# Performance work log

Measured on AMD Instinct MI355X. Metric: run time of the kernel, lower is better.

The kernel has to match this reference:

```python
import jax, jax.numpy as jnp
import numpy as np

N, C_IN, C_OUT = 8192, 256, 128
NEG_SLOPE = 0.2


def setup_inputs() -> dict:
    key = jax.random.key(0)
    k0, k1, k2, k3, k4 = jax.random.split(key, 5)
    x = jax.random.normal(k0, (N, C_IN), dtype=jnp.float32)
    # sparse-ish binary dense adjacency, avg degree ~32
    adj = (jax.random.uniform(k1, (N, N)) < (32.0 / N)).astype(jnp.float32)
    W = jax.random.normal(k2, (C_IN, C_OUT), dtype=jnp.float32) * 0.05
    att_src = jax.random.normal(k3, (C_OUT,), dtype=jnp.float32) * 0.1
    att_dst = jax.random.normal(k4, (C_OUT,), dtype=jnp.float32) * 0.1
    bias = jnp.zeros((C_OUT,), dtype=jnp.float32)
    return {"x": x, "adj": adj, "W": W, "att_src": att_src,
            "att_dst": att_dst, "bias": bias}


def reference(x, adj, W, att_src, att_dst, bias):
    n = adj.shape[0]
    idx = jnp.arange(n)
    adj = adj.at[idx, idx].set(1.0)          # add self loops
    h = x @ W                                 # [N, C_out]
    a_src = h @ att_src                       # [N]
    a_dst = h @ att_dst                       # [N]
    alpha = a_src[:, None] + a_dst[None, :]   # [N, N]
    alpha = jax.nn.leaky_relu(alpha, NEG_SLOPE)
    alpha = adj * jnp.exp(alpha)              # masked exp
    alpha = alpha / alpha.sum(axis=0, keepdims=True)  # column-normalize (dim=0)
    out = (adj * alpha).T @ h + bias          # [N, C_out]
    return out
```

## Files before the change

### kernel.cpp

```cpp
#include <hip/hip_runtime.h>
#include <hip/hip_bf16.h>

#define NN 8192
#define CIN 256
#define COUT 128
#define GR 32
#define GKT 64
#define CH 16
#define ICH (NN / CH)
#define KT 64
#define HTS 72

typedef unsigned short u16;
typedef _Float16 f16;
typedef __attribute__((ext_vector_type(8))) short short8;
typedef __attribute__((ext_vector_type(8))) _Float16 f16x8;
typedef __attribute__((ext_vector_type(16))) float f32x16;

__device__ __forceinline__ short8 pack8_bf16(const float* v) {
    union { __hip_bfloat162 b2[4]; short8 s; } u;
    #pragma unroll
    for (int q = 0; q < 4; ++q)
        u.b2[q] = __float22bfloat162_rn(make_float2(v[2 * q], v[2 * q + 1]));
    return u.s;
}

__global__ __launch_bounds__(256) void adj2mask(const float* __restrict__ adj,
                                                unsigned int* __restrict__ maskT) {
    int tid = threadIdx.x;
    int lane = tid & 63, w = tid >> 6;
    int i = blockIdx.x * 4 + w;
    const float4* rowp = (const float4*)(adj + (size_t)i * NN);
    int half = lane >> 5, slot = lane & 3;
    bool writer = (lane & 31) < 4;
    for (int it = 0; it < 32; it += 8) {
        float4 v[8];
        #pragma unroll
        for (int q = 0; q < 8; ++q)
            v[q] = rowp[(it + q) * 64 + lane];
        #pragma unroll
        for (int q = 0; q < 8; ++q) {
            unsigned long long b0 = __ballot(v[q].x != 0.f);
            unsigned long long b1 = __ballot(v[q].y != 0.f);
            unsigned long long b2 = __ballot(v[q].z != 0.f);
            unsigned long long b3 = __ballot(v[q].w != 0.f);
            unsigned long long bb = slot == 0 ? b0 : slot == 1 ? b1
                                  : slot == 2 ? b2 : b3;
            unsigned int mw = (unsigned int)(bb >> (half * 32));
            int jb = (it + q) * 2 + half;
            if (writer)
                maskT[((size_t)jb * NN + i) * 4 + slot] = mw;
        }
    }
}

__global__ __launch_bounds__(256) void gemm_h(const float* __restrict__ x,
                                              const float* __restrict__ W,
                                              const float* __restrict__ att_src,
                                              const float* __restrict__ att_dst,
                                              u16* __restrict__ h_t,
                                              float* __restrict__ a_src,
                                              float* __restrict__ a_dst) {
    __shared__ float Wt[GKT * COUT];
    __shared__ float xt[GKT][GR + 4];
    __shared__ float ot[GR][COUT + 4];
    int tid = threadIdx.x;
    int i0 = blockIdx.x * GR;
    int tx = tid & 31, ty = tid >> 5;
    int c0 = tx * 4, r0 = ty * 4;
    int xr = tid >> 3, xk = (tid & 7) * 8;
    float acc[4][4] = {};

    for (int kt = 0; kt < CIN; kt += GKT) {
        float4 wv[8];
        #pragma unroll
        for (int j = 0; j < 8; ++j) {
            int f = j * 256 + tid;
            wv[j] = *(const float4*)&W[(size_t)(kt + (f >> 5)) * COUT + (f & 31) * 4];
        }
        float4 xv0 = *(const float4*)&x[(size_t)(i0 + xr) * CIN + kt + xk];
        float4 xv1 = *(const float4*)&x[(size_t)(i0 + xr) * CIN + kt + xk + 4];
        __syncthreads();
        #pragma unroll
        for (int j = 0; j < 8; ++j)
            *(float4*)&Wt[(j * 256 + tid) * 4] = wv[j];
        xt[xk + 0][xr] = xv0.x; xt[xk + 1][xr] = xv0.y;
        xt[xk + 2][xr] = xv0.z; xt[xk + 3][xr] = xv0.w;
        xt[xk + 4][xr] = xv1.x; xt[xk + 5][xr] = xv1.y;
        xt[xk + 6][xr] = xv1.z; xt[xk + 7][xr] = xv1.w;
        __syncthreads();
        #pragma unroll 8
        for (int k = 0; k < GKT; ++k) {
            float4 wk = *(const float4*)&Wt[k * COUT + c0];
            float4 xf = *(const float4*)&xt[k][r0];
            float xa[4] = {xf.x, xf.y, xf.z, xf.w};
            #pragma unroll
            for (int a = 0; a < 4; ++a) {
                acc[a][0] += xa[a] * wk.x; acc[a][1] += xa[a] * wk.y;
                acc[a][2] += xa[a] * wk.z; acc[a][3] += xa[a] * wk.w;
            }
        }
    }

    float4 asv = *(const float4*)&att_src[c0];
    float4 adv = *(const float4*)&att_dst[c0];
    #pragma unroll
    for (int a = 0; a < 4; ++a) {
        float4 o = make_float4(acc[a][0], acc[a][1], acc[a][2], acc[a][3]);
        *(float4*)&ot[r0 + a][c0] = o;
        float s = o.x * asv.x + o.y * asv.y + o.z * asv.z + o.w * asv.w;
        float d = o.x * adv.x + o.y * adv.y + o.z * adv.z + o.w * adv.w;
        #pragma unroll
        for (int m = 16; m >= 1; m >>= 1) {
            s += __shfl_xor(s, m, 32);
            d += __shfl_xor(d, m, 32);
        }
        if (tx == 0) {
            a_src[i0 + r0 + a] = s;
            a_dst[i0 + r0 + a] = d;
        }
    }
    __syncthreads();
    int c = tid >> 1, hf = tid & 1;
    float vals[16];
    #pragma unroll
    for (int q = 0; q < 16; ++q) vals[q] = ot[hf * 16 + q][c];
    *(short8*)(h_t + (size_t)c * NN + i0 + hf * 16)     = pack8_bf16(vals);
    *(short8*)(h_t + (size_t)c * NN + i0 + hf * 16 + 8) = pack8_bf16(vals + 8);
}

__global__ __launch_bounds__(256, 3) void gat_mm(const unsigned int* __restrict__ maskT,
                                                 const u16* __restrict__ h_t,
                                                 const float* __restrict__ a_src,
                                                 const float* __restrict__ a_dst,
                                                 f16* __restrict__ pout,
                                                 float* __restrict__ pden) {
    __shared__ unsigned int maskS[KT * 4];
    __shared__ u16 htS[128 * HTS];
    __shared__ float asrcS[ICH];
    int tid = threadIdx.x;
    int lane = tid & 63, w = tid >> 6;
    int jb = blockIdx.x & 63, ch = blockIdx.x >> 6;
    int j0 = jb * 128;
    int i0 = ch * ICH;
    int half = lane >> 5;
    int jloc = w * 32 + (lane & 31);
    int gj = j0 + jloc;
    int slot = lane & 3;
    int kbit = jloc >> 2;
    float dj = a_dst[gj];
    if (tid < ICH / 4)
        ((float4*)asrcS)[tid] = ((const float4*)(a_src + i0))[tid];

    f32x16 acc[4];
    #pragma unroll
    for (int nt = 0; nt < 4; ++nt)
        #pragma unroll
        for (int q = 0; q < 16; ++q) acc[nt][q] = 0.f;
    float dsum = 0.f;
    __syncthreads();

    for (int s = 0; s < ICH / KT; ++s) {
        int ib = i0 + s * KT;
        unsigned int mword = maskT[((size_t)jb * NN + ib) * 4 + tid];
        short8 bv[4]; int bc[4], bi[4];
        #pragma unroll
        for (int q = 0; q < 4; ++q) {
            int p = q * 256 + tid;
            bc[q] = p >> 3; bi[q] = (p & 7) * 8;
            bv[q] = *(const short8*)(h_t + (size_t)bc[q] * NN + ib + bi[q]);
        }
        maskS[tid] = mword;
        #pragma unroll
        for (int q = 0; q < 4; ++q)
            *(short8*)(htS + bc[q] * HTS + bi[q]) = bv[q];
        __syncthreads();

        #pragma unroll
        for (int kk = 0; kk < 4; ++kk) {
            int kb = kk * 16 + half * 8;
            int gib = ib + kb;
            short8 bf[4];
            #pragma unroll
            for (int nt = 0; nt < 4; ++nt)
                bf[nt] = *(const short8*)(htS + (nt * 32 + (lane & 31)) * HTS + kb);
            float pv[8];
            #pragma unroll
            for (int e = 0; e < 8; ++e) {
                unsigned int mw = maskS[(kb + e) * 4 + slot];
                float t = asrcS[s * KT + kb + e] + dj;
                float ev = __expf(fmaxf(t, 0.2f * t));
                bool on = ((mw >> kbit) & 1u) | (gib + e == gj);
                pv[e] = on ? ev : 0.f;
                dsum += pv[e];
            }
            short8 af = pack8_bf16(pv);
            #pragma unroll
            for (int nt = 0; nt < 4; ++nt)
                acc[nt] = __builtin_amdgcn_mfma_f32_32x32x16_bf16(af, bf[nt],
                                                                  acc[nt], 0, 0, 0);
        }
        __syncthreads();
    }

    #pragma unroll
    for (int nt = 0; nt < 4; ++nt) {
        int c = nt * 32 + (lane & 31);
        #pragma unroll
        for (int r = 0; r < 16; ++r) {
            int row = (r & 3) + 8 * (r >> 2) + 4 * half;
            int j = j0 + w * 32 + row;
            pout[((size_t)ch * NN + j) * COUT + c] = (f16)acc[nt][r];
        }
    }
    float dall = dsum + __shfl_xor(dsum, 32, 64);
    if (half == 0) pden[(size_t)ch * NN + gj] = dall;
}

__global__ __launch_bounds__(256) void gat_reduce(const f16* __restrict__ pout,
                                                  const float* __restrict__ pden,
                                                  const float* __restrict__ bias,
                                                  float* __restrict__ out) {
    int idx = blockIdx.x * 256 + threadIdx.x;
    int j = idx >> 4;
    int c8 = (idx & 15) * 8;
    float den = 0.f;
    #pragma unroll
    for (int ch = 0; ch < CH; ++ch) den += pden[(size_t)ch * NN + j];
    float s[8] = {};
    #pragma unroll
    for (int ch = 0; ch < CH; ++ch) {
        f16x8 pv = *(const f16x8*)(pout + ((size_t)ch * NN + j) * COUT + c8);
        #pragma unroll
        for (int q = 0; q < 8; ++q) s[q] += (float)pv[q];
    }
    float inv = 1.0f / den;
    float4 b0 = *(const float4*)&bias[c8];
    float4 b1 = *(const float4*)&bias[c8 + 4];
    float4 o0 = make_float4(s[0] * inv + b0.x, s[1] * inv + b0.y,
                            s[2] * inv + b0.z, s[3] * inv + b0.w);
    float4 o1 = make_float4(s[4] * inv + b1.x, s[5] * inv + b1.y,
                            s[6] * inv + b1.z, s[7] * inv + b1.w);
    *(float4*)&out[(size_t)j * COUT + c8]     = o0;
    *(float4*)&out[(size_t)j * COUT + c8 + 4] = o1;
}

extern "C" void kernel_launch(void* const* d_in, const int* in_sizes, int n_in,
                              void* d_out, int out_size, void* d_ws, size_t ws_size,
                              hipStream_t stream) {
    const float* x       = (const float*)d_in[0];
    const float* adj     = (const float*)d_in[1];
    const float* W       = (const float*)d_in[2];
    const float* att_src = (const float*)d_in[3];
    const float* att_dst = (const float*)d_in[4];
    const float* bias    = (const float*)d_in[5];
    float* out = (float*)d_out;

    u16*   h_t   = (u16*)d_ws;
    float* a_src = (float*)((char*)d_ws + (size_t)2 * 1024 * 1024);
    float* a_dst = a_src + NN;
    float* pden  = a_dst + NN;
    unsigned int* maskT = (unsigned int*)(pden + (size_t)CH * NN);
    f16*   pout  = (f16*)(maskT + (size_t)64 * NN * 4);

    adj2mask  <<<NN / 4, 256, 0, stream>>>(adj, maskT);
    gemm_h    <<<NN / GR, 256, 0, stream>>>(x, W, att_src, att_dst, h_t, a_src, a_dst);
    gat_mm    <<<64 * CH, 256, 0, stream>>>(maskT, h_t, a_src, a_dst, pout, pden);
    gat_reduce<<<NN * COUT / 8 / 256, 256, 0, stream>>>(pout, pden, bias, out);
}
```

Measured before the change: 436.6 us.

## Widen gat_mm blocks to 512 columns and store mask row-major via LDS staging

The mask kernel now stages ballot words in shared memory and writes each adjacency row's bitmask as contiguous 256-word rows, instead of scattered transposed stores. gat_mm grows to 1024-thread blocks covering 512 output columns, so each staged h tile and mask slice is shared by 16 waves rather than 4. The mask slice is padded to stride 17, and the loop moves its barrier to before the LDS stores. The aim is to cut redundant global loads of h_t and to get coalesced mask writes. The cost is fewer, larger blocks (256) and a heavier register and occupancy demand.

```diff
diff --git a/kernel.cpp b/kernel.cpp
--- a/kernel.cpp
+++ b/kernel.cpp
@@ -26,31 +26,32 @@
 }
 
 __global__ __launch_bounds__(256) void adj2mask(const float* __restrict__ adj,
-                                                unsigned int* __restrict__ maskT) {
+                                                unsigned int* __restrict__ maskR) {
+    __shared__ unsigned int buf[4][64];
     int tid = threadIdx.x;
     int lane = tid & 63, w = tid >> 6;
     int i = blockIdx.x * 4 + w;
     const float4* rowp = (const float4*)(adj + (size_t)i * NN);
-    int half = lane >> 5, slot = lane & 3;
-    bool writer = (lane & 31) < 4;
-    for (int it = 0; it < 32; it += 8) {
+    for (int t = 0; t < 4; ++t) {
         float4 v[8];
         #pragma unroll
         for (int q = 0; q < 8; ++q)
-            v[q] = rowp[(it + q) * 64 + lane];
+            v[q] = rowp[t * 512 + q * 64 + lane];
         #pragma unroll
         for (int q = 0; q < 8; ++q) {
             unsigned long long b0 = __ballot(v[q].x != 0.f);
             unsigned long long b1 = __ballot(v[q].y != 0.f);
             unsigned long long b2 = __ballot(v[q].z != 0.f);
             unsigned long long b3 = __ballot(v[q].w != 0.f);
-            unsigned long long bb = slot == 0 ? b0 : slot == 1 ? b1
-                                  : slot == 2 ? b2 : b3;
-            unsigned int mw = (unsigned int)(bb >> (half * 32));
-            int jb = (it + q) * 2 + half;
-            if (writer)
-                maskT[((size_t)jb * NN + i) * 4 + slot] = mw;
-        }
+            if (lane < 8) {
+                int s_ = lane & 3, h_ = lane >> 2;
+                unsigned long long bb = s_ == 0 ? b0 : s_ == 1 ? b1
+                                      : s_ == 2 ? b2 : b3;
+                buf[w][q * 8 + h_ * 4 + s_] = (unsigned int)(bb >> (h_ * 32));
+            }
+        }
+        unsigned int word = buf[w][lane];
+        maskR[(size_t)i * 256 + t * 64 + lane] = word;
     }
 }
 
@@ -129,25 +130,25 @@
     *(short8*)(h_t + (size_t)c * NN + i0 + hf * 16 + 8) = pack8_bf16(vals + 8);
 }
 
-__global__ __launch_bounds__(256, 3) void gat_mm(const unsigned int* __restrict__ maskT,
-                                                 const u16* __restrict__ h_t,
-                                                 const float* __restrict__ a_src,
-                                                 const float* __restrict__ a_dst,
-                                                 f16* __restrict__ pout,
-                                                 float* __restrict__ pden) {
-    __shared__ unsigned int maskS[KT * 4];
+__global__ __launch_bounds__(1024, 4) void gat_mm(const unsigned int* __restrict__ maskR,
+                                                  const u16* __restrict__ h_t,
+                                                  const float* __restrict__ a_src,
+                                                  const float* __restrict__ a_dst,
+                                                  f16* __restrict__ pout,
+                                                  float* __restrict__ pden) {
+    __shared__ unsigned int maskS[KT * 17];
     __shared__ u16 htS[128 * HTS];
     __shared__ float asrcS[ICH];
     int tid = threadIdx.x;
     int lane = tid & 63, w = tid >> 6;
-    int jb = blockIdx.x & 63, ch = blockIdx.x >> 6;
-    int j0 = jb * 128;
+    int jb = blockIdx.x & 15, ch = blockIdx.x >> 4;
+    int j0 = jb * 512;
     int i0 = ch * ICH;
-    int half = lane >> 5;
-    int jloc = w * 32 + (lane & 31);
+    int half = lane >> 5, l = lane & 31;
+    int jloc = w * 32 + l;
     int gj = j0 + jloc;
-    int slot = lane & 3;
-    int kbit = jloc >> 2;
+    int Wloc = (w >> 3) * 8 + ((w >> 2) & 1) * 4 + (l & 3);
+    int kbit = (w & 3) * 8 + (l >> 2);
     float dj = a_dst[gj];
     if (tid < ICH / 4)
         ((float4*)asrcS)[tid] = ((const float4*)(a_src + i0))[tid];
@@ -160,20 +161,15 @@
     float dsum = 0.f;
     __syncthreads();
 
+    int mi = tid >> 4, mw_ = tid & 15;
+    int bc = tid >> 3, bchunk = (tid & 7) * 8;
     for (int s = 0; s < ICH / KT; ++s) {
         int ib = i0 + s * KT;
-        unsigned int mword = maskT[((size_t)jb * NN + ib) * 4 + tid];
-        short8 bv[4]; int bc[4], bi[4];
-        #pragma unroll
-        for (int q = 0; q < 4; ++q) {
-            int p = q * 256 + tid;
-            bc[q] = p >> 3; bi[q] = (p & 7) * 8;
-            bv[q] = *(const short8*)(h_t + (size_t)bc[q] * NN + ib + bi[q]);
-        }
-        maskS[tid] = mword;
-        #pragma unroll
-        for (int q = 0; q < 4; ++q)
-            *(short8*)(htS + bc[q] * HTS + bi[q]) = bv[q];
+        unsigned int mword = maskR[(size_t)(ib + mi) * 256 + jb * 16 + mw_];
+        short8 bv = *(const short8*)(h_t + (size_t)bc * NN + ib + bchunk);
+        __syncthreads();
+        maskS[mi * 17 + mw_] = mword;
+        *(short8*)(htS + bc * HTS + bchunk) = bv;
         __syncthreads();
 
         #pragma unroll
@@ -183,11 +179,11 @@
             short8 bf[4];
             #pragma unroll
             for (int nt = 0; nt < 4; ++nt)
-                bf[nt] = *(const short8*)(htS + (nt * 32 + (lane & 31)) * HTS + kb);
+                bf[nt] = *(const short8*)(htS + (nt * 32 + l) * HTS + kb);
             float pv[8];
             #pragma unroll
             for (int e = 0; e < 8; ++e) {
-                unsigned int mw = maskS[(kb + e) * 4 + slot];
+                unsigned int mw = maskS[(kb + e) * 17 + Wloc];
                 float t = asrcS[s * KT + kb + e] + dj;
                 float ev = __expf(fmaxf(t, 0.2f * t));
                 bool on = ((mw >> kbit) & 1u) | (gib + e == gj);
@@ -200,12 +196,11 @@
                 acc[nt] = __builtin_amdgcn_mfma_f32_32x32x16_bf16(af, bf[nt],
                                                                   acc[nt], 0, 0, 0);
         }
-        __syncthreads();
     }
 
     #pragma unroll
     for (int nt = 0; nt < 4; ++nt) {
-        int c = nt * 32 + (lane & 31);
+        int c = nt * 32 + l;
         #pragma unroll
         for (int r = 0; r < 16; ++r) {
             int row = (r & 3) + 8 * (r >> 2) + 4 * half;
@@ -260,11 +255,11 @@
     float* a_src = (float*)((char*)d_ws + (size_t)2 * 1024 * 1024);
     float* a_dst = a_src + NN;
     float* pden  = a_dst + NN;
-    unsigned int* maskT = (unsigned int*)(pden + (size_t)CH * NN);
-    f16*   pout  = (f16*)(maskT + (size_t)64 * NN * 4);
-
-    adj2mask  <<<NN / 4, 256, 0, stream>>>(adj, maskT);
+    unsigned int* maskR = (unsigned int*)(pden + (size_t)CH * NN);
+    f16*   pout  = (f16*)(maskR + (size_t)NN * 256);
+
+    adj2mask  <<<NN / 4, 256, 0, stream>>>(adj, maskR);
     gemm_h    <<<NN / GR, 256, 0, stream>>>(x, W, att_src, att_dst, h_t, a_src, a_dst);
-    gat_mm    <<<64 * CH, 256, 0, stream>>>(maskT, h_t, a_src, a_dst, pout, pden);
+    gat_mm    <<<256, 1024, 0, stream>>>(maskR, h_t, a_src, a_dst, pout, pden);
     gat_reduce<<<NN * COUT / 8 / 256, 256, 0, stream>>>(pout, pden, bias, out);
 }
```

After: 434.5 us. Within noise of the previous version (-0.5%).
